# Kernel optimization log

Measured on AMD Instinct MI355X. Metric: run time of the kernel, lower is better.

Reference implementation:

```python
import jax, jax.numpy as jnp
import numpy as np

C_S, C_Z, N_HEADS = 768, 64, 12
HEAD_DIM = C_S // N_HEADS
L = 1024
EPS = 1e-5


def _ln(x, g, b):
    mu = jnp.mean(x, axis=-1, keepdims=True)
    var = jnp.mean((x - mu) ** 2, axis=-1, keepdims=True)
    return (x - mu) * jax.lax.rsqrt(var + EPS) * g + b


def setup_inputs() -> dict:
    key = jax.random.key(0)
    ks = jax.random.split(key, 12)
    w = lambda k, shp, fan_in: jax.random.normal(k, shp, dtype=jnp.float32) / np.sqrt(fan_in)
    return {
        "single": jax.random.normal(ks[0], (L, C_S), dtype=jnp.float32),
        "pair": jax.random.normal(ks[1], (L, L, C_Z), dtype=jnp.float32),
        "ln_s_g": jnp.ones((C_S,), jnp.float32),
        "ln_s_b": jnp.zeros((C_S,), jnp.float32),
        "ln_z_g": jnp.ones((C_Z,), jnp.float32),
        "ln_z_b": jnp.zeros((C_Z,), jnp.float32),
        "Wq": w(ks[2], (C_S, C_S), C_S),
        "Wk": w(ks[3], (C_S, C_S), C_S),
        "Wv": w(ks[4], (C_S, C_S), C_S),
        "Wb": w(ks[5], (C_Z, N_HEADS), C_Z),
        "Wout": w(ks[6], (C_S, C_S), C_S),
        "bout": jnp.zeros((C_S,), jnp.float32),
        "Wgate": w(ks[7], (C_S, C_S), C_S),
        "bgate": jnp.zeros((C_S,), jnp.float32),
    }


def reference(single, pair, ln_s_g, ln_s_b, ln_z_g, ln_z_b,
              Wq, Wk, Wv, Wb, Wout, bout, Wgate, bgate):
    Lq = single.shape[0]
    s = _ln(single, ln_s_g, ln_s_b)                    # [L, C_S]
    z = _ln(pair, ln_z_g, ln_z_b)                      # [L, L, C_Z]
    q = (s @ Wq).reshape(Lq, N_HEADS, HEAD_DIM)
    k = (s @ Wk).reshape(Lq, N_HEADS, HEAD_DIM)
    v = (s @ Wv).reshape(Lq, N_HEADS, HEAD_DIM)
    logits = jnp.einsum('ihd,jhd->hij', q, k) / np.sqrt(HEAD_DIM)
    logits = logits + jnp.einsum('ijc,ch->hij', z, Wb)  # pair bias per head
    attn = jax.nn.softmax(logits, axis=-1)              # [H, L, L]
    out = jnp.einsum('hij,jhd->ihd', attn, v).reshape(Lq, C_S)
    return single + jax.nn.sigmoid(s @ Wgate + bgate) * (out @ Wout + bout)
```

## Files before the change

### kernel.cpp

```cpp
#include <hip/hip_runtime.h>

#define LQ 1024
#define CS 768
#define CZ 64
#define NH 12
#define HD 64

typedef float4 f4;
using bf16x8 = __attribute__((ext_vector_type(8))) short;
using f32x4  = __attribute__((ext_vector_type(4))) float;

static __device__ __forceinline__ unsigned short f2bf(float f) {
  unsigned int u = __float_as_uint(f);
  u += 0x7fffu + ((u >> 16) & 1u);
  return (unsigned short)(u >> 16);
}
static __device__ __forceinline__ float bf2f(unsigned short b) {
  return __uint_as_float(((unsigned int)b) << 16);
}

__global__ __launch_bounds__(256) void ln_wconv_k(
    const float* __restrict__ x, const float* __restrict__ g,
    const float* __restrict__ b, unsigned short* __restrict__ s_out,
    const float* __restrict__ Wq, const float* __restrict__ Wk,
    const float* __restrict__ Wv, const float* __restrict__ Wg,
    const float* __restrict__ Wo, unsigned short* __restrict__ wt) {
  const int bid = blockIdx.x;
  const int t = threadIdx.x;
  if (bid < LQ) {
    const int row = bid;
    const float* xr = x + (size_t)row * CS;
    float v0 = xr[t], v1 = xr[t + 256], v2 = xr[t + 512];
    float s1 = v0 + v1 + v2;
    float s2 = v0 * v0 + v1 * v1 + v2 * v2;
#pragma unroll
    for (int m = 1; m < 64; m <<= 1) {
      s1 += __shfl_xor(s1, m);
      s2 += __shfl_xor(s2, m);
    }
    __shared__ float r1[4], r2[4];
    const int wid = t >> 6;
    if ((t & 63) == 0) { r1[wid] = s1; r2[wid] = s2; }
    __syncthreads();
    s1 = r1[0] + r1[1] + r1[2] + r1[3];
    s2 = r2[0] + r2[1] + r2[2] + r2[3];
    const float mu = s1 * (1.f / CS);
    const float var = s2 * (1.f / CS) - mu * mu;
    const float rs = rsqrtf(var + 1e-5f);
    s_out[(size_t)row * CS + t]       = f2bf((v0 - mu) * rs * g[t]       + b[t]);
    s_out[(size_t)row * CS + t + 256] = f2bf((v1 - mu) * rs * g[t + 256] + b[t + 256]);
    s_out[(size_t)row * CS + t + 512] = f2bf((v2 - mu) * rs * g[t + 512] + b[t + 512]);
  } else {
    int r = bid - LQ;
    const int bz = r / 144; r %= 144;
    const int n0 = (r % 12) * 64, k0 = (r / 12) * 64;
    const float* W;
    switch (bz) {
      case 0: W = Wq; break;
      case 1: W = Wk; break;
      case 2: W = Wv; break;
      case 3: W = Wg; break;
      default: W = Wo; break;
    }
    unsigned short* o = wt + (size_t)bz * CS * CS;
    __shared__ float T[64][68];
    {
      const int rr = t >> 4, c = (t & 15) * 4;
#pragma unroll
      for (int u = 0; u < 4; ++u) {
        const f4 v = *(const f4*)&W[(size_t)(k0 + rr + u * 16) * CS + n0 + c];
        *(f4*)&T[rr + u * 16][c] = v;
      }
    }
    __syncthreads();
    {
      const int rn = t >> 2, ck = (t & 3) * 16;
      __align__(16) unsigned short tmp[16];
#pragma unroll
      for (int u = 0; u < 16; ++u) tmp[u] = f2bf(T[ck + u][rn]);
      unsigned short* dst = &o[(size_t)(n0 + rn) * CS + k0 + ck];
      *(uint4*)dst = ((const uint4*)tmp)[0];
      *(uint4*)(dst + 8) = ((const uint4*)tmp)[1];
    }
  }
}

__global__ __launch_bounds__(256) void qkvg_pair_k(
    const unsigned short* __restrict__ s, const unsigned short* __restrict__ wt,
    const float* __restrict__ bg,
    unsigned short* __restrict__ qb, unsigned short* __restrict__ kb,
    unsigned short* __restrict__ vt, float* __restrict__ gpre,
    const float* __restrict__ pair, const float* __restrict__ zg,
    const float* __restrict__ zb, const float* __restrict__ Wb,
    unsigned short* __restrict__ biasF) {
  __shared__ __align__(16) unsigned short sm[64 * 88 + 128 * 88];
  const int bid = blockIdx.x;
  const int t = threadIdx.x;
  const int w = t >> 6, lane = t & 63, g = lane >> 4, c = lane & 15;

  if (bid < 384) {
    unsigned short (*As)[88] = (unsigned short (*)[88])sm;
    unsigned short (*Bs)[88] = (unsigned short (*)[88])(sm + 64 * 88);
    const int wm = w >> 1, wn = w & 1;
    const int bx = bid % 24, by = bid / 24;
    const int m0 = by * 64;
    const int wid = bx / 6;
    const int nl0 = (bx % 6) * 128;
    const unsigned short* B = wt + (size_t)wid * CS * CS;

    f32x4 acc[2][4];
#pragma unroll
    for (int i = 0; i < 2; ++i)
#pragma unroll
      for (int j = 0; j < 4; ++j) acc[i][j] = (f32x4){0.f, 0.f, 0.f, 0.f};

    const int sra = t >> 2, sha = (t & 3) * 16;
    const int srb = t >> 1, shb = (t & 1) * 32;
    for (int kt = 0; kt < CS; kt += 64) {
      __syncthreads();
#pragma unroll
      for (int u = 0; u < 2; ++u)
        *(uint4*)&As[sra][sha + u * 8] = *(const uint4*)&s[(size_t)(m0 + sra) * CS + kt + sha + u * 8];
#pragma unroll
      for (int u = 0; u < 4; ++u)
        *(uint4*)&Bs[srb][shb + u * 8] = *(const uint4*)&B[(size_t)(nl0 + srb) * CS + kt + shb + u * 8];
      __syncthreads();
#pragma unroll
      for (int kk = 0; kk < 64; kk += 32) {
        bf16x8 af[2], bfr[4];
#pragma unroll
        for (int i = 0; i < 2; ++i) af[i] = *(const bf16x8*)&As[wm * 32 + i * 16 + c][kk + g * 8];
#pragma unroll
        for (int j = 0; j < 4; ++j) bfr[j] = *(const bf16x8*)&Bs[wn * 64 + j * 16 + c][kk + g * 8];
#pragma unroll
        for (int i = 0; i < 2; ++i)
#pragma unroll
          for (int j = 0; j < 4; ++j)
            acc[i][j] = __builtin_amdgcn_mfma_f32_16x16x32_bf16(af[i], bfr[j], acc[i][j], 0, 0, 0);
      }
    }
#pragma unroll
    for (int i = 0; i < 2; ++i) {
#pragma unroll
      for (int j = 0; j < 4; ++j) {
        const int mb = m0 + wm * 32 + i * 16 + g * 4;
        const int nn = nl0 + wn * 64 + j * 16 + c;
        const f32x4 a = acc[i][j];
        if (wid == 0) {
#pragma unroll
          for (int r = 0; r < 4; ++r) qb[(size_t)(mb + r) * CS + nn] = f2bf(a[r] * 0.125f);
        } else if (wid == 1) {
#pragma unroll
          for (int r = 0; r < 4; ++r) kb[(size_t)(mb + r) * CS + nn] = f2bf(a[r]);
        } else if (wid == 2) {
          ushort4 pk;
          pk.x = f2bf(a[0]); pk.y = f2bf(a[1]); pk.z = f2bf(a[2]); pk.w = f2bf(a[3]);
          *(ushort4*)&vt[(size_t)nn * LQ + mb] = pk;
        } else {
          const float bb = bg[nn];
#pragma unroll
          for (int r = 0; r < 4; ++r) gpre[(size_t)(mb + r) * CS + nn] = a[r] + bb;
        }
      }
    }
  } else {
    const int pid = bid - 384;
    const int i0 = (pid >> 2) * 4;
    const int j0 = (pid & 3) * 256;

    float zgr[16], zbr[16];
    *(f4*)&zgr[0]  = *(const f4*)&zg[g * 8];
    *(f4*)&zgr[4]  = *(const f4*)&zg[g * 8 + 4];
    *(f4*)&zgr[8]  = *(const f4*)&zg[32 + g * 8];
    *(f4*)&zgr[12] = *(const f4*)&zg[32 + g * 8 + 4];
    *(f4*)&zbr[0]  = *(const f4*)&zb[g * 8];
    *(f4*)&zbr[4]  = *(const f4*)&zb[g * 8 + 4];
    *(f4*)&zbr[8]  = *(const f4*)&zb[32 + g * 8];
    *(f4*)&zbr[12] = *(const f4*)&zb[32 + g * 8 + 4];

    bf16x8 wf0, wf1;
    const int csafe = (c < NH) ? c : 0;
#pragma unroll
    for (int u = 0; u < 8; ++u) {
      const float w0 = (c < NH) ? Wb[(g * 8 + u) * NH + csafe] : 0.f;
      const float w1 = (c < NH) ? Wb[(32 + g * 8 + u) * NH + csafe] : 0.f;
      wf0[u] = (short)f2bf(w0);
      wf1[u] = (short)f2bf(w1);
    }

    const int il = c & 3, jl = c >> 2;
    const int irow = i0 + il;
    const int gi = i0 >> 4, ga = (i0 >> 2) & 3;
    const size_t hd_base = ((size_t)gi * 16) * 4 * 256 + (size_t)ga * 64;

    auto ldx = [&](int it, float* x0, float* x1) {
      const int jw = j0 + w * 64 + it * 4;
      const float* src = pair + ((size_t)irow * LQ + (jw + jl)) * CZ;
      *(f4*)&x0[0] = *(const f4*)&src[g * 8];
      *(f4*)&x0[4] = *(const f4*)&src[g * 8 + 4];
      *(f4*)&x1[0] = *(const f4*)&src[32 + g * 8];
      *(f4*)&x1[4] = *(const f4*)&src[32 + g * 8 + 4];
    };
    auto proc = [&](int it, const float* x0, const float* x1) {
      float s1 = (((x0[0] + x0[1]) + (x0[2] + x0[3])) + ((x0[4] + x0[5]) + (x0[6] + x0[7])))
               + (((x1[0] + x1[1]) + (x1[2] + x1[3])) + ((x1[4] + x1[5]) + (x1[6] + x1[7])));
      float s2 = (((x0[0]*x0[0] + x0[1]*x0[1]) + (x0[2]*x0[2] + x0[3]*x0[3]))
               +  ((x0[4]*x0[4] + x0[5]*x0[5]) + (x0[6]*x0[6] + x0[7]*x0[7])))
               + (((x1[0]*x1[0] + x1[1]*x1[1]) + (x1[2]*x1[2] + x1[3]*x1[3]))
               +  ((x1[4]*x1[4] + x1[5]*x1[5]) + (x1[6]*x1[6] + x1[7]*x1[7])));
      s1 += __shfl_xor(s1, 16); s1 += __shfl_xor(s1, 32);
      s2 += __shfl_xor(s2, 16); s2 += __shfl_xor(s2, 32);
      const float mu = s1 * (1.f / CZ);
      const float var = s2 * (1.f / CZ) - mu * mu;
      const float rs = rsqrtf(var + 1e-5f);

      bf16x8 a0, a1;
#pragma unroll
      for (int u = 0; u < 8; ++u) {
        a0[u] = (short)f2bf((x0[u] - mu) * rs * zgr[u] + zbr[u]);
        a1[u] = (short)f2bf((x1[u] - mu) * rs * zgr[8 + u] + zbr[8 + u]);
      }

      f32x4 dd = (f32x4){0.f, 0.f, 0.f, 0.f};
      dd = __builtin_amdgcn_mfma_f32_16x16x32_bf16(a0, wf0, dd, 0, 0, 0);
      dd = __builtin_amdgcn_mfma_f32_16x16x32_bf16(a1, wf1, dd, 0, 0, 0);

      if (c < NH) {
        const int jj = j0 + w * 64 + it * 4 + g;
        const size_t base = ((size_t)c * 64) * 16384
                          + hd_base
                          + (size_t)(jj >> 6) * 1024
                          + (size_t)((jj >> 4) & 3) * 256
                          + (jj & 15) * 4;
        ushort4 st;
        st.x = f2bf(dd[0]); st.y = f2bf(dd[1]); st.z = f2bf(dd[2]); st.w = f2bf(dd[3]);
        *(ushort4*)&biasF[base] = st;
      }
    };

    float xa0[8], xa1[8], xb0[8], xb1[8];
    ldx(0, xa0, xa1);
    for (int ip = 0; ip < 8; ++ip) {
      ldx(2 * ip + 1, xb0, xb1);
      proc(2 * ip, xa0, xa1);
      if (ip < 7) ldx(2 * ip + 2, xa0, xa1);
      proc(2 * ip + 1, xb0, xb1);
    }
  }
}

__global__ __launch_bounds__(256) void attn_k(
    const unsigned short* __restrict__ q, const unsigned short* __restrict__ k,
    const unsigned short* __restrict__ vt, const unsigned short* __restrict__ biasF,
    float* __restrict__ Opart, float* __restrict__ ml) {
  __shared__ __align__(16) unsigned short Qs[64][88];
  __shared__ __align__(16) unsigned short Ks[2][64][88];
  __shared__ __align__(16) unsigned short Vts[2][64][88];
  __shared__ __align__(16) unsigned short Ps[4][16][88];
  const int bx = blockIdx.x, h = blockIdx.y, z = blockIdx.z;
  const int i0 = bx * 64;
  const int jb = z * 512;
  const int t = threadIdx.x;
  const int w = t >> 6, lane = t & 63, g = lane >> 4, c = lane & 15;
  const int sr = t >> 2, sc = (t & 3) * 16;

#pragma unroll
  for (int u = 0; u < 2; ++u) {
    *(uint4*)&Qs[sr][sc + u * 8]     = *(const uint4*)&q[(size_t)(i0 + sr) * CS + h * HD + sc + u * 8];
    *(uint4*)&Ks[0][sr][sc + u * 8]  = *(const uint4*)&k[(size_t)(jb + sr) * CS + h * HD + sc + u * 8];
    *(uint4*)&Vts[0][sr][sc + u * 8] = *(const uint4*)&vt[(size_t)(h * HD + sr) * LQ + jb + sc + u * 8];
  }
  const size_t bbase = ((((size_t)h * 64 + (bx * 4 + w)) * 16 + (size_t)z * 8) * 4) * 256 + lane * 4;
  ushort4 bcur[4];
#pragma unroll
  for (int nb = 0; nb < 4; ++nb) bcur[nb] = *(const ushort4*)&biasF[bbase + nb * 256];
  __syncthreads();

  const bf16x8 aq0 = *(const bf16x8*)&Qs[w * 16 + c][g * 8];
  const bf16x8 aq1 = *(const bf16x8*)&Qs[w * 16 + c][32 + g * 8];

  f32x4 acc_o[4];
#pragma unroll
  for (int nb = 0; nb < 4; ++nb) acc_o[nb] = (f32x4){0.f, 0.f, 0.f, 0.f};
  float m_run[4] = {-1e30f, -1e30f, -1e30f, -1e30f};
  float l_run[4] = {0.f, 0.f, 0.f, 0.f};

  for (int jt = 0; jt < 8; ++jt) {
    const int cur = jt & 1;
    uint4 kr0, kr1, vr0, vr1;
    ushort4 bnx[4];
    if (jt < 7) {
      const int jn = jb + (jt + 1) * 64;
      kr0 = *(const uint4*)&k[(size_t)(jn + sr) * CS + h * HD + sc];
      kr1 = *(const uint4*)&k[(size_t)(jn + sr) * CS + h * HD + sc + 8];
      vr0 = *(const uint4*)&vt[(size_t)(h * HD + sr) * LQ + jn + sc];
      vr1 = *(const uint4*)&vt[(size_t)(h * HD + sr) * LQ + jn + sc + 8];
#pragma unroll
      for (int nb = 0; nb < 4; ++nb)
        bnx[nb] = *(const ushort4*)&biasF[bbase + (size_t)(jt + 1) * 1024 + nb * 256];
    }

    f32x4 sa[4];
#pragma unroll
    for (int nb = 0; nb < 4; ++nb) {
      f32x4 ci;
      ci[0] = bf2f(bcur[nb].x); ci[1] = bf2f(bcur[nb].y);
      ci[2] = bf2f(bcur[nb].z); ci[3] = bf2f(bcur[nb].w);
      const bf16x8 b0 = *(const bf16x8*)&Ks[cur][nb * 16 + c][g * 8];
      const bf16x8 b1 = *(const bf16x8*)&Ks[cur][nb * 16 + c][32 + g * 8];
      ci = __builtin_amdgcn_mfma_f32_16x16x32_bf16(aq0, b0, ci, 0, 0, 0);
      ci = __builtin_amdgcn_mfma_f32_16x16x32_bf16(aq1, b1, ci, 0, 0, 0);
      sa[nb] = ci;
    }

    float mt[4];
#pragma unroll
    for (int r = 0; r < 4; ++r) {
      float v = fmaxf(fmaxf(sa[0][r], sa[1][r]), fmaxf(sa[2][r], sa[3][r]));
      v = fmaxf(v, __shfl_xor(v, 1));
      v = fmaxf(v, __shfl_xor(v, 2));
      v = fmaxf(v, __shfl_xor(v, 4));
      v = fmaxf(v, __shfl_xor(v, 8));
      mt[r] = v;
    }
    float scale[4], ps[4];
#pragma unroll
    for (int r = 0; r < 4; ++r) {
      const float mn = fmaxf(m_run[r], mt[r]);
      scale[r] = __expf(m_run[r] - mn);
      m_run[r] = mn;
      ps[r] = 0.f;
    }
#pragma unroll
    for (int nb = 0; nb < 4; ++nb) {
#pragma unroll
      for (int r = 0; r < 4; ++r) {
        const float p = __expf(sa[nb][r] - m_run[r]);
        ps[r] += p;
        Ps[w][g * 4 + r][nb * 16 + c] = f2bf(p);
      }
    }
#pragma unroll
    for (int r = 0; r < 4; ++r) {
      float v = ps[r];
      v += __shfl_xor(v, 1);
      v += __shfl_xor(v, 2);
      v += __shfl_xor(v, 4);
      v += __shfl_xor(v, 8);
      l_run[r] = l_run[r] * scale[r] + v;
#pragma unroll
      for (int nb = 0; nb < 4; ++nb) acc_o[nb][r] *= scale[r];
    }

#pragma unroll
    for (int kb = 0; kb < 2; ++kb) {
      const bf16x8 pa = *(const bf16x8*)&Ps[w][c][kb * 32 + g * 8];
#pragma unroll
      for (int nb = 0; nb < 4; ++nb) {
        const bf16x8 bv = *(const bf16x8*)&Vts[cur][nb * 16 + c][kb * 32 + g * 8];
        acc_o[nb] = __builtin_amdgcn_mfma_f32_16x16x32_bf16(pa, bv, acc_o[nb], 0, 0, 0);
      }
    }

    if (jt < 7) {
      *(uint4*)&Ks[cur ^ 1][sr][sc]      = kr0;
      *(uint4*)&Ks[cur ^ 1][sr][sc + 8]  = kr1;
      *(uint4*)&Vts[cur ^ 1][sr][sc]     = vr0;
      *(uint4*)&Vts[cur ^ 1][sr][sc + 8] = vr1;
      __syncthreads();
#pragma unroll
      for (int nb = 0; nb < 4; ++nb) bcur[nb] = bnx[nb];
    }
  }

  const size_t rowb = (size_t)(z * NH + h) * LQ + i0 + w * 16 + g * 4;
#pragma unroll
  for (int nb = 0; nb < 4; ++nb)
#pragma unroll
    for (int r = 0; r < 4; ++r)
      Opart[(rowb + r) * HD + nb * 16 + c] = acc_o[nb][r];
  if (c == 0) {
#pragma unroll
    for (int r = 0; r < 4; ++r) {
      ml[(rowb + r) * 2]     = m_run[r];
      ml[(rowb + r) * 2 + 1] = l_run[r];
    }
  }
}

__global__ __launch_bounds__(256) void combine_k(
    const float* __restrict__ Opart, const float* __restrict__ ml,
    unsigned short* __restrict__ attno) {
  const int t = threadIdx.x;
  const int row = blockIdx.x * 4 + (t >> 6);
  const int d = t & 63;
  const int h = row >> 10, i = row & 1023;
  const size_t r0 = (size_t)h * LQ + i;
  const size_t r1 = (size_t)(NH + h) * LQ + i;
  const float m0 = ml[r0 * 2], l0 = ml[r0 * 2 + 1];
  const float m1 = ml[r1 * 2], l1 = ml[r1 * 2 + 1];
  const float M = fmaxf(m0, m1);
  const float a0 = __expf(m0 - M), a1 = __expf(m1 - M);
  const float L = a0 * l0 + a1 * l1;
  const float o = (a0 * Opart[r0 * HD + d] + a1 * Opart[r1 * HD + d]) / L;
  attno[(size_t)i * CS + h * HD + d] = f2bf(o);
}

__global__ __launch_bounds__(256) void gemm_final_k(
    const unsigned short* __restrict__ A, const unsigned short* __restrict__ wt,
    const float* __restrict__ bout, const float* __restrict__ single,
    const float* __restrict__ gpre, float* __restrict__ out) {
  __shared__ __align__(16) unsigned short As[64][88];
  __shared__ __align__(16) unsigned short Bs[128][88];
  const int t = threadIdx.x;
  const int wave = t >> 6, lane = t & 63, g = lane >> 4, c = lane & 15;
  const int wm = wave >> 1, wn = wave & 1;
  const int m0 = blockIdx.y * 64;
  const int nl0 = blockIdx.x * 128;
  const unsigned short* B = wt + (size_t)4 * CS * CS;

  f32x4 acc[2][4];
#pragma unroll
  for (int i = 0; i < 2; ++i)
#pragma unroll
    for (int j = 0; j < 4; ++j) acc[i][j] = (f32x4){0.f, 0.f, 0.f, 0.f};

  const int sra = t >> 2, sha = (t & 3) * 16;
  const int srb = t >> 1, shb = (t & 1) * 32;
  for (int kt = 0; kt < CS; kt += 64) {
    __syncthreads();
#pragma unroll
    for (int u = 0; u < 2; ++u)
      *(uint4*)&As[sra][sha + u * 8] = *(const uint4*)&A[(size_t)(m0 + sra) * CS + kt + sha + u * 8];
#pragma unroll
    for (int u = 0; u < 4; ++u)
      *(uint4*)&Bs[srb][shb + u * 8] = *(const uint4*)&B[(size_t)(nl0 + srb) * CS + kt + shb + u * 8];
    __syncthreads();
#pragma unroll
    for (int kk = 0; kk < 64; kk += 32) {
      bf16x8 af[2], bfr[4];
#pragma unroll
      for (int i = 0; i < 2; ++i) af[i] = *(const bf16x8*)&As[wm * 32 + i * 16 + c][kk + g * 8];
#pragma unroll
      for (int j = 0; j < 4; ++j) bfr[j] = *(const bf16x8*)&Bs[wn * 64 + j * 16 + c][kk + g * 8];
#pragma unroll
      for (int i = 0; i < 2; ++i)
#pragma unroll
        for (int j = 0; j < 4; ++j)
          acc[i][j] = __builtin_amdgcn_mfma_f32_16x16x32_bf16(af[i], bfr[j], acc[i][j], 0, 0, 0);
    }
  }

#pragma unroll
  for (int i = 0; i < 2; ++i) {
#pragma unroll
    for (int j = 0; j < 4; ++j) {
      const int mb = m0 + wm * 32 + i * 16 + g * 4;
      const int nn = nl0 + wn * 64 + j * 16 + c;
      const float bb = bout[nn];
      const f32x4 a = acc[i][j];
#pragma unroll
      for (int r = 0; r < 4; ++r) {
        const size_t idx = (size_t)(mb + r) * CS + nn;
        const float gate = 1.f / (1.f + __expf(-gpre[idx]));
        out[idx] = single[idx] + gate * (a[r] + bb);
      }
    }
  }
}

extern "C" void kernel_launch(void* const* d_in, const int* in_sizes, int n_in,
                              void* d_out, int out_size, void* d_ws, size_t ws_size,
                              hipStream_t stream) {
  const float* single = (const float*)d_in[0];
  const float* pair   = (const float*)d_in[1];
  const float* ln_s_g = (const float*)d_in[2];
  const float* ln_s_b = (const float*)d_in[3];
  const float* ln_z_g = (const float*)d_in[4];
  const float* ln_z_b = (const float*)d_in[5];
  const float* Wq     = (const float*)d_in[6];
  const float* Wk     = (const float*)d_in[7];
  const float* Wv     = (const float*)d_in[8];
  const float* Wb     = (const float*)d_in[9];
  const float* Wout   = (const float*)d_in[10];
  const float* bout   = (const float*)d_in[11];
  const float* Wgate  = (const float*)d_in[12];
  const float* bgate  = (const float*)d_in[13];
  float* out = (float*)d_out;

  unsigned short* s_bf  = (unsigned short*)d_ws;
  unsigned short* wt    = s_bf  + (size_t)LQ * CS;
  unsigned short* q_bf  = wt    + (size_t)5 * CS * CS;
  unsigned short* k_bf  = q_bf  + (size_t)LQ * CS;
  unsigned short* vt_bf = k_bf  + (size_t)LQ * CS;
  unsigned short* attno = vt_bf + (size_t)CS * LQ;
  unsigned short* biasF = attno + (size_t)LQ * CS;
  float* gpre  = (float*)(biasF + (size_t)NH * LQ * LQ);
  float* Opart = gpre  + (size_t)LQ * CS;
  float* mlw   = Opart + (size_t)2 * NH * LQ * HD;

  hipLaunchKernelGGL(ln_wconv_k, dim3(LQ + 720), dim3(256), 0, stream,
                     single, ln_s_g, ln_s_b, s_bf, Wq, Wk, Wv, Wgate, Wout, wt);
  hipLaunchKernelGGL(qkvg_pair_k, dim3(384 + 1024), dim3(256), 0, stream,
                     s_bf, wt, bgate, q_bf, k_bf, vt_bf, gpre,
                     pair, ln_z_g, ln_z_b, Wb, biasF);
  hipLaunchKernelGGL(attn_k, dim3(16, NH, 2), dim3(256), 0, stream,
                     q_bf, k_bf, vt_bf, biasF, Opart, mlw);
  hipLaunchKernelGGL(combine_k, dim3(3072), dim3(256), 0, stream,
                     Opart, mlw, attno);
  hipLaunchKernelGGL(gemm_final_k, dim3(6, 16), dim3(256), 0, stream,
                     attno, wt, bout, single, gpre, out);
}
```

Baseline: 123.2 us.

## Shrink QKVG GEMM k-tile to 32 and stream pair reads with nontemporal loads

The QKVG GEMM branch now stages 32-wide k-slices in LDS instead of 64, with a padded row stride of 40. This shrinks shared memory per block and may raise occupancy, but it doubles the number of barrier-separated iterations. The pair-LayerNorm branch is rewritten as a fully unrolled, double-buffered loop that loads pair data with nontemporal loads, so the single-use stream does not pollute the caches. Gamma and beta are held in vector registers, and the computation itself is unchanged.

Result: slower. 136.6 us (+10.9%).

```diff
diff --git a/kernel.cpp b/kernel.cpp
--- a/kernel.cpp
+++ b/kernel.cpp
@@ -93,14 +93,14 @@
     const float* __restrict__ pair, const float* __restrict__ zg,
     const float* __restrict__ zb, const float* __restrict__ Wb,
     unsigned short* __restrict__ biasF) {
-  __shared__ __align__(16) unsigned short sm[64 * 88 + 128 * 88];
+  __shared__ __align__(16) unsigned short sm[192 * 40];
   const int bid = blockIdx.x;
   const int t = threadIdx.x;
   const int w = t >> 6, lane = t & 63, g = lane >> 4, c = lane & 15;
 
   if (bid < 384) {
-    unsigned short (*As)[88] = (unsigned short (*)[88])sm;
-    unsigned short (*Bs)[88] = (unsigned short (*)[88])(sm + 64 * 88);
+    unsigned short (*As)[40] = (unsigned short (*)[40])sm;
+    unsigned short (*Bs)[40] = (unsigned short (*)[40])(sm + 64 * 40);
     const int wm = w >> 1, wn = w & 1;
     const int bx = bid % 24, by = bid / 24;
     const int m0 = by * 64;
@@ -114,30 +114,24 @@
 #pragma unroll
       for (int j = 0; j < 4; ++j) acc[i][j] = (f32x4){0.f, 0.f, 0.f, 0.f};
 
-    const int sra = t >> 2, sha = (t & 3) * 16;
-    const int srb = t >> 1, shb = (t & 1) * 32;
-    for (int kt = 0; kt < CS; kt += 64) {
+    const int sra = t >> 2, sha = (t & 3) * 8;
+    const int srb = t >> 1, shb = (t & 1) * 16;
+    for (int kt = 0; kt < CS; kt += 32) {
       __syncthreads();
-#pragma unroll
-      for (int u = 0; u < 2; ++u)
-        *(uint4*)&As[sra][sha + u * 8] = *(const uint4*)&s[(size_t)(m0 + sra) * CS + kt + sha + u * 8];
-#pragma unroll
-      for (int u = 0; u < 4; ++u)
-        *(uint4*)&Bs[srb][shb + u * 8] = *(const uint4*)&B[(size_t)(nl0 + srb) * CS + kt + shb + u * 8];
+      *(uint4*)&As[sra][sha]     = *(const uint4*)&s[(size_t)(m0 + sra) * CS + kt + sha];
+      *(uint4*)&Bs[srb][shb]     = *(const uint4*)&B[(size_t)(nl0 + srb) * CS + kt + shb];
+      *(uint4*)&Bs[srb][shb + 8] = *(const uint4*)&B[(size_t)(nl0 + srb) * CS + kt + shb + 8];
       __syncthreads();
-#pragma unroll
-      for (int kk = 0; kk < 64; kk += 32) {
-        bf16x8 af[2], bfr[4];
-#pragma unroll
-        for (int i = 0; i < 2; ++i) af[i] = *(const bf16x8*)&As[wm * 32 + i * 16 + c][kk + g * 8];
-#pragma unroll
-        for (int j = 0; j < 4; ++j) bfr[j] = *(const bf16x8*)&Bs[wn * 64 + j * 16 + c][kk + g * 8];
-#pragma unroll
-        for (int i = 0; i < 2; ++i)
-#pragma unroll
-          for (int j = 0; j < 4; ++j)
-            acc[i][j] = __builtin_amdgcn_mfma_f32_16x16x32_bf16(af[i], bfr[j], acc[i][j], 0, 0, 0);
-      }
+      bf16x8 af[2], bfr[4];
+#pragma unroll
+      for (int i = 0; i < 2; ++i) af[i] = *(const bf16x8*)&As[wm * 32 + i * 16 + c][g * 8];
+#pragma unroll
+      for (int j = 0; j < 4; ++j) bfr[j] = *(const bf16x8*)&Bs[wn * 64 + j * 16 + c][g * 8];
+#pragma unroll
+      for (int i = 0; i < 2; ++i)
+#pragma unroll
+        for (int j = 0; j < 4; ++j)
+          acc[i][j] = __builtin_amdgcn_mfma_f32_16x16x32_bf16(af[i], bfr[j], acc[i][j], 0, 0, 0);
     }
 #pragma unroll
     for (int i = 0; i < 2; ++i) {
@@ -167,16 +161,16 @@
     const int pid = bid - 384;
     const int i0 = (pid >> 2) * 4;
     const int j0 = (pid & 3) * 256;
-
-    float zgr[16], zbr[16];
-    *(f4*)&zgr[0]  = *(const f4*)&zg[g * 8];
-    *(f4*)&zgr[4]  = *(const f4*)&zg[g * 8 + 4];
-    *(f4*)&zgr[8]  = *(const f4*)&zg[32 + g * 8];
-    *(f4*)&zgr[12] = *(const f4*)&zg[32 + g * 8 + 4];
-    *(f4*)&zbr[0]  = *(const f4*)&zb[g * 8];
-    *(f4*)&zbr[4]  = *(const f4*)&zb[g * 8 + 4];
-    *(f4*)&zbr[8]  = *(const f4*)&zb[32 + g * 8];
-    *(f4*)&zbr[12] = *(const f4*)&zb[32 + g * 8 + 4];
+    const int il = c & 3, jl = c >> 2;
+    const int irow = i0 + il;
+    const int g2 = g * 2;
+    const int gi = i0 >> 4, ga = (i0 >> 2) & 3;
+    const size_t hd_base = ((size_t)gi * 16) * 4 * 256 + (size_t)ga * 64;
+
+    const f32x4* zgp = (const f32x4*)zg;
+    const f32x4* zbp = (const f32x4*)zb;
+    const f32x4 zg0a = zgp[g2], zg0b = zgp[g2 + 1], zg1a = zgp[g2 + 8], zg1b = zgp[g2 + 9];
+    const f32x4 zb0a = zbp[g2], zb0b = zbp[g2 + 1], zb1a = zbp[g2 + 8], zb1b = zbp[g2 + 9];
 
     bf16x8 wf0, wf1;
     const int csafe = (c < NH) ? c : 0;
@@ -188,42 +182,70 @@
       wf1[u] = (short)f2bf(w1);
     }
 
-    const int il = c & 3, jl = c >> 2;
-    const int irow = i0 + il;
-    const int gi = i0 >> 4, ga = (i0 >> 2) & 3;
-    const size_t hd_base = ((size_t)gi * 16) * 4 * 256 + (size_t)ga * 64;
-
-    auto ldx = [&](int it, float* x0, float* x1) {
-      const int jw = j0 + w * 64 + it * 4;
-      const float* src = pair + ((size_t)irow * LQ + (jw + jl)) * CZ;
-      *(f4*)&x0[0] = *(const f4*)&src[g * 8];
-      *(f4*)&x0[4] = *(const f4*)&src[g * 8 + 4];
-      *(f4*)&x1[0] = *(const f4*)&src[32 + g * 8];
-      *(f4*)&x1[4] = *(const f4*)&src[32 + g * 8 + 4];
-    };
-    auto proc = [&](int it, const float* x0, const float* x1) {
-      float s1 = (((x0[0] + x0[1]) + (x0[2] + x0[3])) + ((x0[4] + x0[5]) + (x0[6] + x0[7])))
-               + (((x1[0] + x1[1]) + (x1[2] + x1[3])) + ((x1[4] + x1[5]) + (x1[6] + x1[7])));
-      float s2 = (((x0[0]*x0[0] + x0[1]*x0[1]) + (x0[2]*x0[2] + x0[3]*x0[3]))
-               +  ((x0[4]*x0[4] + x0[5]*x0[5]) + (x0[6]*x0[6] + x0[7]*x0[7])))
-               + (((x1[0]*x1[0] + x1[1]*x1[1]) + (x1[2]*x1[2] + x1[3]*x1[3]))
-               +  ((x1[4]*x1[4] + x1[5]*x1[5]) + (x1[6]*x1[6] + x1[7]*x1[7])));
+    f32x4 p00, p01, p02, p03;
+    f32x4 p10, p11, p12, p13;
+    {
+      const f32x4* s0 = (const f32x4*)(pair + ((size_t)irow * LQ + (j0 + w * 64 + jl)) * CZ);
+      p00 = __builtin_nontemporal_load(&s0[g2]);
+      p01 = __builtin_nontemporal_load(&s0[g2 + 1]);
+      p02 = __builtin_nontemporal_load(&s0[g2 + 8]);
+      p03 = __builtin_nontemporal_load(&s0[g2 + 9]);
+    }
+#pragma unroll
+    for (int it = 0; it < 16; ++it) {
+      const bool useA = (it & 1) == 0;
+      if (it < 15) {
+        const f32x4* sn = (const f32x4*)(pair + ((size_t)irow * LQ + (j0 + w * 64 + (it + 1) * 4 + jl)) * CZ);
+        if (useA) {
+          p10 = __builtin_nontemporal_load(&sn[g2]);
+          p11 = __builtin_nontemporal_load(&sn[g2 + 1]);
+          p12 = __builtin_nontemporal_load(&sn[g2 + 8]);
+          p13 = __builtin_nontemporal_load(&sn[g2 + 9]);
+        } else {
+          p00 = __builtin_nontemporal_load(&sn[g2]);
+          p01 = __builtin_nontemporal_load(&sn[g2 + 1]);
+          p02 = __builtin_nontemporal_load(&sn[g2 + 8]);
+          p03 = __builtin_nontemporal_load(&sn[g2 + 9]);
+        }
+      }
+      const f32x4 x0a = useA ? p00 : p10;
+      const f32x4 x0b = useA ? p01 : p11;
+      const f32x4 x1a = useA ? p02 : p12;
+      const f32x4 x1b = useA ? p03 : p13;
+
+      float s1 = (((x0a[0] + x0a[1]) + (x0a[2] + x0a[3])) + ((x0b[0] + x0b[1]) + (x0b[2] + x0b[3])))
+               + (((x1a[0] + x1a[1]) + (x1a[2] + x1a[3])) + ((x1b[0] + x1b[1]) + (x1b[2] + x1b[3])));
+      float s2 = (((x0a[0]*x0a[0] + x0a[1]*x0a[1]) + (x0a[2]*x0a[2] + x0a[3]*x0a[3]))
+               +  ((x0b[0]*x0b[0] + x0b[1]*x0b[1]) + (x0b[2]*x0b[2] + x0b[3]*x0b[3])))
+               + (((x1a[0]*x1a[0] + x1a[1]*x1a[1]) + (x1a[2]*x1a[2] + x1a[3]*x1a[3]))
+               +  ((x1b[0]*x1b[0] + x1b[1]*x1b[1]) + (x1b[2]*x1b[2] + x1b[3]*x1b[3])));
       s1 += __shfl_xor(s1, 16); s1 += __shfl_xor(s1, 32);
       s2 += __shfl_xor(s2, 16); s2 += __shfl_xor(s2, 32);
       const float mu = s1 * (1.f / CZ);
       const float var = s2 * (1.f / CZ) - mu * mu;
       const float rs = rsqrtf(var + 1e-5f);
 
-      bf16x8 a0, a1;
-#pragma unroll
-      for (int u = 0; u < 8; ++u) {
-        a0[u] = (short)f2bf((x0[u] - mu) * rs * zgr[u] + zbr[u]);
-        a1[u] = (short)f2bf((x1[u] - mu) * rs * zgr[8 + u] + zbr[8 + u]);
-      }
+      bf16x8 pa, pb;
+      pa[0] = (short)f2bf((x0a[0] - mu) * rs * zg0a[0] + zb0a[0]);
+      pa[1] = (short)f2bf((x0a[1] - mu) * rs * zg0a[1] + zb0a[1]);
+      pa[2] = (short)f2bf((x0a[2] - mu) * rs * zg0a[2] + zb0a[2]);
+      pa[3] = (short)f2bf((x0a[3] - mu) * rs * zg0a[3] + zb0a[3]);
+      pa[4] = (short)f2bf((x0b[0] - mu) * rs * zg0b[0] + zb0b[0]);
+      pa[5] = (short)f2bf((x0b[1] - mu) * rs * zg0b[1] + zb0b[1]);
+      pa[6] = (short)f2bf((x0b[2] - mu) * rs * zg0b[2] + zb0b[2]);
+      pa[7] = (short)f2bf((x0b[3] - mu) * rs * zg0b[3] + zb0b[3]);
+      pb[0] = (short)f2bf((x1a[0] - mu) * rs * zg1a[0] + zb1a[0]);
+      pb[1] = (short)f2bf((x1a[1] - mu) * rs * zg1a[1] + zb1a[1]);
+      pb[2] = (short)f2bf((x1a[2] - mu) * rs * zg1a[2] + zb1a[2]);
+      pb[3] = (short)f2bf((x1a[3] - mu) * rs * zg1a[3] + zb1a[3]);
+      pb[4] = (short)f2bf((x1b[0] - mu) * rs * zg1b[0] + zb1b[0]);
+      pb[5] = (short)f2bf((x1b[1] - mu) * rs * zg1b[1] + zb1b[1]);
+      pb[6] = (short)f2bf((x1b[2] - mu) * rs * zg1b[2] + zb1b[2]);
+      pb[7] = (short)f2bf((x1b[3] - mu) * rs * zg1b[3] + zb1b[3]);
 
       f32x4 dd = (f32x4){0.f, 0.f, 0.f, 0.f};
-      dd = __builtin_amdgcn_mfma_f32_16x16x32_bf16(a0, wf0, dd, 0, 0, 0);
-      dd = __builtin_amdgcn_mfma_f32_16x16x32_bf16(a1, wf1, dd, 0, 0, 0);
+      dd = __builtin_amdgcn_mfma_f32_16x16x32_bf16(pa, wf0, dd, 0, 0, 0);
+      dd = __builtin_amdgcn_mfma_f32_16x16x32_bf16(pb, wf1, dd, 0, 0, 0);
 
       if (c < NH) {
         const int jj = j0 + w * 64 + it * 4 + g;
@@ -236,15 +258,6 @@
         st.x = f2bf(dd[0]); st.y = f2bf(dd[1]); st.z = f2bf(dd[2]); st.w = f2bf(dd[3]);
         *(ushort4*)&biasF[base] = st;
       }
-    };
-
-    float xa0[8], xa1[8], xb0[8], xb1[8];
-    ldx(0, xa0, xa1);
-    for (int ip = 0; ip < 8; ++ip) {
-      ldx(2 * ip + 1, xb0, xb1);
-      proc(2 * ip, xa0, xa1);
-      if (ip < 7) ldx(2 * ip + 2, xa0, xa1);
-      proc(2 * ip + 1, xb0, xb1);
     }
   }
 }
```
